# Kernel optimization log

Measured on AMD Instinct MI355X. Metric: run time of the kernel, lower is better.

The kernel has to match this reference:

```python
import jax, jax.numpy as jnp
import numpy as np

B, T, V, D, H, C = 256, 512, 400000, 50, 50, 5  # batch, seq, vocab, emb_dim, lstm_hidden, classes


def setup_inputs() -> dict:
    key = jax.random.key(0)
    ks = jax.random.split(key, 9)
    x = jax.random.randint(ks[0], (B, T), 0, V)
    lengths = jax.random.randint(ks[1], (B,), 1, T + 1)
    bows = jnp.zeros((B, 1), dtype=jnp.float32)  # unused by the model
    emb_table = jax.random.normal(ks[2], (V, D), dtype=jnp.float32) * 0.1
    s = 1.0 / np.sqrt(H)
    W_ih = jax.random.uniform(ks[3], (4 * H, D), minval=-s, maxval=s, dtype=jnp.float32)
    W_hh = jax.random.uniform(ks[4], (4 * H, H), minval=-s, maxval=s, dtype=jnp.float32)
    b_ih = jax.random.uniform(ks[5], (4 * H,), minval=-s, maxval=s, dtype=jnp.float32)
    b_hh = jax.random.uniform(ks[6], (4 * H,), minval=-s, maxval=s, dtype=jnp.float32)
    sl = 1.0 / np.sqrt(3 * H)
    W_lin = jax.random.uniform(ks[7], (C, 3 * H), minval=-sl, maxval=sl, dtype=jnp.float32)
    b_lin = jax.random.uniform(ks[8], (C,), minval=-sl, maxval=sl, dtype=jnp.float32)
    return {"x": x, "lengths": lengths, "bows": bows, "emb_table": emb_table,
            "W_ih": W_ih, "W_hh": W_hh, "b_ih": b_ih, "b_hh": b_hh,
            "W_lin": W_lin, "b_lin": b_lin}


def _lstm(emb, W_ih, W_hh, b_ih, b_hh):
    # emb: [B,T,D] -> h_all: [B,T,H]; PyTorch gate order i,f,g,o
    xp = jnp.einsum('btd,gd->btg', emb, W_ih) + b_ih + b_hh  # [B,T,4H]
    xp_t = jnp.swapaxes(xp, 0, 1)  # [T,B,4H]
    h0 = jnp.zeros((emb.shape[0], W_hh.shape[1]), emb.dtype)
    c0 = jnp.zeros_like(h0)

    def step(carry, xt):
        h, c = carry
        g = xt + h @ W_hh.T
        i, f, gg, o = jnp.split(g, 4, axis=-1)
        i, f, o = jax.nn.sigmoid(i), jax.nn.sigmoid(f), jax.nn.sigmoid(o)
        c = f * c + i * jnp.tanh(gg)
        h = o * jnp.tanh(c)
        return (h, c), h

    _, h_all = jax.lax.scan(step, (h0, c0), xp_t)
    return jnp.swapaxes(h_all, 0, 1)  # [B,T,H]


def reference(x, lengths, bows, emb_table, W_ih, W_hh, b_ih, b_hh, W_lin, b_lin):
    emb = emb_table[x]                              # [B,T,D]
    h_all = _lstm(emb, W_ih, W_hh, b_ih, b_hh)      # [B,T,H]
    idx = jnp.minimum(lengths, h_all.shape[1]) - 1  # last valid timestep
    last = jnp.take_along_axis(h_all, idx[:, None, None], axis=1)[:, 0, :]  # [B,H]
    # faithful to original: sum over full padded seq / length, max over full padded seq
    mean = jnp.sum(emb, axis=1) / lengths[:, None].astype(emb.dtype)        # [B,D]
    mx = jnp.max(emb, axis=1)                                               # [B,D]
    rep = jnp.concatenate([last, mean, mx], axis=1)                          # [B,3H]
    return rep @ W_lin.T + b_lin
```

## Files before the change

### kernel.cpp

```cpp
#include <hip/hip_runtime.h>
#include <cmath>

#define NB 256
#define NT 512
#define ND 50
#define NH 50
#define NC 5

typedef float f32x4 __attribute__((ext_vector_type(4)));
typedef float f32x2 __attribute__((ext_vector_type(2)));

__device__ __forceinline__ float rcpf(float x) { return __builtin_amdgcn_rcpf(x); }
__device__ __forceinline__ float rdl(float v, int l) {
    return __int_as_float(__builtin_amdgcn_readlane(__float_as_int(v), l));
}
__device__ __forceinline__ void gload4(f32x4& d, const float* p) {
    asm volatile("global_load_dwordx4 %0, %1, off" : "=v"(d) : "v"(p));
}

#define FENCE_BAR                                             \
    asm volatile("s_waitcnt lgkmcnt(0)" ::: "memory");        \
    __builtin_amdgcn_s_barrier();                             \
    asm volatile("" ::: "memory");

__global__ __launch_bounds__(256)
void k0_prep(const float* __restrict__ W_hh, const float* __restrict__ W_ih,
             float* __restrict__ wsWih, float* __restrict__ wsWhh)
{
    int idx = blockIdx.x * 256 + threadIdx.x;
    if (idx < 200 * 52) {
        int d = idx / 52, c = idx - (idx / 52) * 52;
        wsWih[idx] = (c < ND) ? W_ih[d * ND + c] : 0.f;
    } else if (idx < 2 * 200 * 52) {
        int j = idx - 200 * 52;
        int d = j / 52, c = j - (j / 52) * 52;
        wsWhh[j] = (c < NH) ? W_hh[d * NH + c] : 0.f;
    }
}

#define DECLROW(P) f32x4 P##_0{},P##_1{},P##_2{},P##_3{},P##_4{},P##_5{},P##_6{},P##_7{}, \
                         P##_8{},P##_9{},P##_10{},P##_11{},P##_12{};
#define LOADROW(P,B) { const float* b_=(B); \
    gload4(P##_0,b_+0);  gload4(P##_1,b_+4);  gload4(P##_2,b_+8);  gload4(P##_3,b_+12); \
    gload4(P##_4,b_+16); gload4(P##_5,b_+20); gload4(P##_6,b_+24); gload4(P##_7,b_+28); \
    gload4(P##_8,b_+32); gload4(P##_9,b_+36); gload4(P##_10,b_+40); gload4(P##_11,b_+44); \
    gload4(P##_12,b_+48); }

#define FMA2(H,W,A) __builtin_elementwise_fma((H),(W),(A))
#define KP2(J) { f32x2 a_=e0[2*(J)], b_=e0[2*(J)+1], c_=e1[2*(J)], d_=e1[2*(J)+1]; \
    A01=FMA2(a_,w##J.xy,A01); A23=FMA2(b_,w##J.zw,A23);                            \
    B01=FMA2(c_,w##J.xy,B01); B23=FMA2(d_,w##J.zw,B23); }

__global__ __launch_bounds__(256)
void k1_xproj(const int* __restrict__ x, const int* __restrict__ lengths,
              const float* __restrict__ emb_table,
              const float* __restrict__ wsWih, const float* __restrict__ b_ih,
              const float* __restrict__ b_hh,
              float* __restrict__ xp, int t0, int t1, int tiles, int tcAlloc)
{
    const int b    = blockIdx.x / tiles;
    const int tile = blockIdx.x % tiles;
    const int rt0  = t0 + tile * 64;
    if (rt0 >= t1) return;
    if (rt0 >= lengths[b]) return;
    const int nrows = min(64, t1 - rt0);

    const int tid = threadIdx.x;
    const int* xrow = x + (size_t)b * NT + rt0;

    float bsum = 0.f;
    const float* wrow = wsWih + tid * 52;
    f32x4 w0{},w1{},w2{},w3{},w4{},w5{},w6{},w7{},w8{},w9{},w10{},w11{},w12{};
    gload4(w0,wrow+0); gload4(w1,wrow+4); gload4(w2,wrow+8); gload4(w3,wrow+12);
    gload4(w4,wrow+16); gload4(w5,wrow+20); gload4(w6,wrow+24); gload4(w7,wrow+28);
    gload4(w8,wrow+32); gload4(w9,wrow+36); gload4(w10,wrow+40); gload4(w11,wrow+44);
    gload4(w12,wrow+48);
    if (tid < 200) bsum = b_ih[tid] + b_hh[tid];
    asm volatile("s_waitcnt vmcnt(0)" ::: "memory");
    __builtin_amdgcn_sched_barrier(0);

    if (tid < 200) {
        const int wr = 4 * (tid % NH) + (tid / NH);
        float* xpb = xp + ((size_t)b * tcAlloc + (rt0 - t0)) * 200 + wr;
        int xr0 = __builtin_amdgcn_readfirstlane(xrow[0]);
        int xr1 = __builtin_amdgcn_readfirstlane(xrow[1]);
        for (int row = 0; row < nrows; row += 2) {
            const f32x2* e0 = (const f32x2*)(emb_table + (size_t)xr0 * ND);
            const f32x2* e1 = (const f32x2*)(emb_table + (size_t)xr1 * ND);
            const int nr = (row + 2 < nrows) ? row + 2 : 0;
            int nx0 = __builtin_amdgcn_readfirstlane(xrow[nr]);
            int nx1 = __builtin_amdgcn_readfirstlane(xrow[nr + 1]);
            f32x2 A01 = {bsum, 0.f}, A23 = {0.f, 0.f};
            f32x2 B01 = {bsum, 0.f}, B23 = {0.f, 0.f};
            KP2(0) KP2(1) KP2(2) KP2(3) KP2(4) KP2(5)
            KP2(6) KP2(7) KP2(8) KP2(9) KP2(10) KP2(11)
            A01 = FMA2(e0[24], w12.xy, A01);
            B01 = FMA2(e1[24], w12.xy, B01);
            xpb[(size_t)row * 200]       = (A01.x + A01.y) + (A23.x + A23.y);
            xpb[(size_t)(row + 1) * 200] = (B01.x + B01.y) + (B23.x + B23.y);
            xr0 = nx0; xr1 = nx1;
        }
    }
}

#define CDOT1(SEED,OUT) { f32x2 A01 = {(SEED), 0.f}, A23 = {0.f, 0.f};        \
    A01=FMA2(hp0 ,CW_0.xy ,A01); A23=FMA2(hp1 ,CW_0.zw ,A23);                 \
    A01=FMA2(hp2 ,CW_1.xy ,A01); A23=FMA2(hp3 ,CW_1.zw ,A23);                 \
    A01=FMA2(hp4 ,CW_2.xy ,A01); A23=FMA2(hp5 ,CW_2.zw ,A23);                 \
    A01=FMA2(hp6 ,CW_3.xy ,A01); A23=FMA2(hp7 ,CW_3.zw ,A23);                 \
    A01=FMA2(hp8 ,CW_4.xy ,A01); A23=FMA2(hp9 ,CW_4.zw ,A23);                 \
    A01=FMA2(hp10,CW_5.xy ,A01); A23=FMA2(hp11,CW_5.zw ,A23);                 \
    A01=FMA2(hp12,CW_6.xy ,A01); A23=FMA2(hp13,CW_6.zw ,A23);                 \
    A01=FMA2(hp14,CW_7.xy ,A01); A23=FMA2(hp15,CW_7.zw ,A23);                 \
    A01=FMA2(hp16,CW_8.xy ,A01); A23=FMA2(hp17,CW_8.zw ,A23);                 \
    A01=FMA2(hp18,CW_9.xy ,A01); A23=FMA2(hp19,CW_9.zw ,A23);                 \
    A01=FMA2(hp20,CW_10.xy,A01); A23=FMA2(hp21,CW_10.zw,A23);                 \
    A01=FMA2(hp22,CW_11.xy,A01); A23=FMA2(hp23,CW_11.zw,A23);                 \
    A23=FMA2(hp24,CW_12.xy,A23);                                              \
    OUT = (A01.x + A01.y) + (A23.x + A23.y); }

#define SSTEP(XQ, S) {                                                        \
    f32x2 hp0 ={rdl(hv,0 ),rdl(hv,1 )}, hp1 ={rdl(hv,2 ),rdl(hv,3 )};         \
    f32x2 hp2 ={rdl(hv,4 ),rdl(hv,5 )}, hp3 ={rdl(hv,6 ),rdl(hv,7 )};         \
    f32x2 hp4 ={rdl(hv,8 ),rdl(hv,9 )}, hp5 ={rdl(hv,10),rdl(hv,11)};         \
    f32x2 hp6 ={rdl(hv,12),rdl(hv,13)}, hp7 ={rdl(hv,14),rdl(hv,15)};         \
    f32x2 hp8 ={rdl(hv,16),rdl(hv,17)}, hp9 ={rdl(hv,18),rdl(hv,19)};         \
    f32x2 hp10={rdl(hv,20),rdl(hv,21)}, hp11={rdl(hv,22),rdl(hv,23)};         \
    f32x2 hp12={rdl(hv,24),rdl(hv,25)}, hp13={rdl(hv,26),rdl(hv,27)};         \
    f32x2 hp14={rdl(hv,28),rdl(hv,29)}, hp15={rdl(hv,30),rdl(hv,31)};         \
    f32x2 hp16={rdl(hv,32),rdl(hv,33)}, hp17={rdl(hv,34),rdl(hv,35)};         \
    f32x2 hp18={rdl(hv,36),rdl(hv,37)}, hp19={rdl(hv,38),rdl(hv,39)};         \
    f32x2 hp20={rdl(hv,40),rdl(hv,41)}, hp21={rdl(hv,42),rdl(hv,43)};         \
    f32x2 hp22={rdl(hv,44),rdl(hv,45)}, hp23={rdl(hv,46),rdl(hv,47)};         \
    f32x2 hp24={rdl(hv,48),rdl(hv,49)};                                       \
    float gg;                                                                 \
    CDOT1(XQ, gg)                                                             \
    { int sn_ = (S) + 4; if (sn_ > nsteps - 1) sn_ = nsteps - 1;              \
      XQ = xpb[(size_t)sn_ * 200]; }                                          \
    float act = fmaf(rcpf(1.f + __expf(-sce * gg)), sce, ade);                \
    abuf[(S) & 1][wid][kln] = act;                                            \
    FENCE_BAR                                                                 \
    float i_ = abuf[(S) & 1][0][kln];                                         \
    float f_ = abuf[(S) & 1][1][kln];                                         \
    float gt = abuf[(S) & 1][2][kln];                                         \
    float o_ = abuf[(S) & 1][3][kln];                                         \
    cst = fmaf(f_, cst, i_ * gt);                                             \
    float th = fmaf(rcpf(1.f + __expf(-2.f * cst)), 2.f, -1.f);               \
    hv = o_ * th;                                                             \
    hkeep = (t0 + (S) == lastidx) ? hv : hkeep;                               \
}

__global__ __launch_bounds__(256)
__attribute__((amdgpu_waves_per_eu(1, 1)))
void k2_scan(const int* __restrict__ x, const int* __restrict__ lengths,
             const float* __restrict__ emb_table,
             const float* __restrict__ wsWhh, const float* __restrict__ xp,
             const float* __restrict__ W_lin, const float* __restrict__ b_lin,
             float* __restrict__ stH, float* __restrict__ stC, float* __restrict__ lastH,
             float* __restrict__ out, int t0, int t1, int tcAlloc)
{
    const int b   = blockIdx.x, tid = threadIdx.x;
    const int wid = tid >> 6;
    const int kln = tid & 63;
    const int kc  = (kln < NH) ? kln : NH - 1;

    __shared__ __align__(16) float abuf[2][4][64];
    __shared__ int xv[NT];
    __shared__ float ps[5][52], pm[5][52];
    __shared__ float rep[160];

    const int lastidx = min(lengths[b], NT) - 1;
    const int nsteps  = t1 - t0;

    float hv  = (t0 == 0) ? 0.f : stH[b * NH + kc];
    float cst = (t0 == 0) ? 0.f : stC[b * NH + kc];

    DECLROW(CW)
    LOADROW(CW, wsWhh + ((size_t)wid * NH + kc) * 52)
    asm volatile("s_waitcnt vmcnt(0)" ::: "memory");
    __builtin_amdgcn_sched_barrier(0);

    const float sce = (wid == 2) ? 2.f : 1.f;
    const float ade = (wid == 2) ? -1.f : 0.f;

    const float* xpb = xp + (size_t)b * tcAlloc * 200 + 4 * kc + wid;
    float xq0 = xpb[0];
    float xq1 = xpb[200];
    float xq2 = xpb[400];
    float xq3 = xpb[600];
    float hkeep = 0.f;

    for (int s4 = 0; s4 < nsteps; s4 += 4) {
        SSTEP(xq0, s4 + 0)
        SSTEP(xq1, s4 + 1)
        SSTEP(xq2, s4 + 2)
        SSTEP(xq3, s4 + 3)
    }

    if (wid == 0 && kln < NH) {
        stH[b * NH + kln] = hv;
        stC[b * NH + kln] = cst;
        if (lastidx >= t0 && lastidx < t1) lastH[b * NH + kln] = hkeep;
    }

    if (t1 == NT) {
        for (int i = tid; i < NT; i += 256) xv[i] = x[(size_t)b * NT + i];
        __syncthreads();
        const int g5 = tid / ND, d5 = tid - g5 * ND;
        if (tid < 250) {
            float s = 0.f, m = -INFINITY;
            #pragma unroll 4
            for (int t = g5; t < NT; t += 5) {
                float e = emb_table[(size_t)xv[t] * ND + d5];
                s += e; m = fmaxf(m, e);
            }
            ps[g5][d5] = s; pm[g5][d5] = m;
        }
        __syncthreads();
        if (tid < NH) {
            float s = ps[0][tid] + ps[1][tid] + ps[2][tid] + ps[3][tid] + ps[4][tid];
            float m = fmaxf(fmaxf(fmaxf(pm[0][tid], pm[1][tid]),
                                  fmaxf(pm[2][tid], pm[3][tid])), pm[4][tid]);
            rep[tid]          = (lastidx >= t0) ? hkeep : lastH[b * NH + tid];
            rep[NH + tid]     = s / (float)lengths[b];
            rep[2 * NH + tid] = m;
        }
        __syncthreads();
        if (tid < NC) {
            float acc = b_lin[tid];
            #pragma unroll 5
            for (int j = 0; j < 3 * NH; ++j)
                acc = fmaf(rep[j], W_lin[tid * 3 * NH + j], acc);
            out[(size_t)b * NC + tid] = acc;
        }
    }
}

extern "C" void kernel_launch(void* const* d_in, const int* in_sizes, int n_in,
                              void* d_out, int out_size, void* d_ws, size_t ws_size,
                              hipStream_t stream) {
    const int*   x     = (const int*)d_in[0];
    const int*   len   = (const int*)d_in[1];
    const float* emb   = (const float*)d_in[3];
    const float* W_ih  = (const float*)d_in[4];
    const float* W_hh  = (const float*)d_in[5];
    const float* b_ih  = (const float*)d_in[6];
    const float* b_hh  = (const float*)d_in[7];
    const float* W_lin = (const float*)d_in[8];
    const float* b_lin = (const float*)d_in[9];
    float* outp = (float*)d_out;

    float* stH   = (float*)d_ws;
    float* stC   = stH + NB * NH;
    float* lastH = stC + NB * NH;
    float* wsWih = (float*)((char*)d_ws + 160 * 1024);
    float* wsWhh = wsWih + 200 * 52;
    const size_t xpOff = 256 * 1024;
    float* xp = (float*)((char*)d_ws + xpOff);

    size_t avail = (ws_size > xpOff + 8192) ? ws_size - xpOff - 8192 : 0;
    int tc = (int)(avail / ((size_t)NB * 200 * sizeof(float)));
    tc &= ~3;
    if (tc > NT) tc = NT;
    if (tc < 4)  tc = 4;

    hipLaunchKernelGGL(k0_prep, dim3(82), dim3(256), 0, stream, W_hh, W_ih, wsWih, wsWhh);

    for (int t0 = 0; t0 < NT; t0 += tc) {
        const int t1 = min(NT, t0 + tc);
        const int tiles = (t1 - t0 + 63) / 64;
        hipLaunchKernelGGL(k1_xproj, dim3(NB * tiles), dim3(256), 0, stream,
                           x, len, emb, wsWih, b_ih, b_hh, xp, t0, t1, tiles, tc);
        hipLaunchKernelGGL(k2_scan, dim3(NB), dim3(256), 0, stream,
                           x, len, emb, wsWhh, xp, W_lin, b_lin,
                           stH, stC, lastH, outp, t0, t1, tc);
    }
}
```

Before: 249.0 us.

## Fuse embedding sum/max pooling into the input-projection kernel

Moves the mean/max pooling over the full padded sequence out of the tail of the serial scan kernel and into the parallel xproj kernel. Idle threads 200-249 of each tile block gather one embedding column per row and write per-tile partial sums and maxes to a workspace buffer. The scan kernel then only reduces the 8 partials. Tiles past the sequence length still launch, so pooling covers padding, but they skip the GEMV. This takes latency off the one-block-per-batch tail, at the cost of extra launched blocks and a larger workspace offset that may shrink the time-chunk size.

After: 256.6 us. 1.03x slower.

```diff
diff --git a/kernel.cpp b/kernel.cpp
--- a/kernel.cpp
+++ b/kernel.cpp
@@ -56,17 +56,21 @@
               const float* __restrict__ emb_table,
               const float* __restrict__ wsWih, const float* __restrict__ b_ih,
               const float* __restrict__ b_hh,
-              float* __restrict__ xp, int t0, int t1, int tiles, int tcAlloc)
+              float* __restrict__ xp, float* __restrict__ pool,
+              int t0, int t1, int tiles, int tcAlloc, int fullPool)
 {
     const int b    = blockIdx.x / tiles;
     const int tile = blockIdx.x % tiles;
     const int rt0  = t0 + tile * 64;
     if (rt0 >= t1) return;
-    if (rt0 >= lengths[b]) return;
+    if (!fullPool && rt0 >= lengths[b]) return;
     const int nrows = min(64, t1 - rt0);
 
     const int tid = threadIdx.x;
     const int* xrow = x + (size_t)b * NT + rt0;
+    const bool doGemv = (tid < 200) && (rt0 < lengths[b]);
+    const bool doPool = fullPool && (tid >= 200) && (tid < 250);
+    const int  pd = tid - 200;
 
     float bsum = 0.f;
     const float* wrow = wsWih + tid * 52;
@@ -79,17 +83,19 @@
     asm volatile("s_waitcnt vmcnt(0)" ::: "memory");
     __builtin_amdgcn_sched_barrier(0);
 
-    if (tid < 200) {
-        const int wr = 4 * (tid % NH) + (tid / NH);
-        float* xpb = xp + ((size_t)b * tcAlloc + (rt0 - t0)) * 200 + wr;
-        int xr0 = __builtin_amdgcn_readfirstlane(xrow[0]);
-        int xr1 = __builtin_amdgcn_readfirstlane(xrow[1]);
-        for (int row = 0; row < nrows; row += 2) {
-            const f32x2* e0 = (const f32x2*)(emb_table + (size_t)xr0 * ND);
-            const f32x2* e1 = (const f32x2*)(emb_table + (size_t)xr1 * ND);
-            const int nr = (row + 2 < nrows) ? row + 2 : 0;
-            int nx0 = __builtin_amdgcn_readfirstlane(xrow[nr]);
-            int nx1 = __builtin_amdgcn_readfirstlane(xrow[nr + 1]);
+    const int wr = 4 * ((tid % NH)) + (tid / NH);
+    float* xpb = xp + ((size_t)b * tcAlloc + (rt0 - t0)) * 200 + wr;
+    float ps = 0.f, pm = -INFINITY;
+
+    int xr0 = __builtin_amdgcn_readfirstlane(xrow[0]);
+    int xr1 = __builtin_amdgcn_readfirstlane(xrow[1]);
+    for (int row = 0; row < nrows; row += 2) {
+        const f32x2* e0 = (const f32x2*)(emb_table + (size_t)xr0 * ND);
+        const f32x2* e1 = (const f32x2*)(emb_table + (size_t)xr1 * ND);
+        const int nr = (row + 2 < nrows) ? row + 2 : 0;
+        int nx0 = __builtin_amdgcn_readfirstlane(xrow[nr]);
+        int nx1 = __builtin_amdgcn_readfirstlane(xrow[nr + 1]);
+        if (doGemv) {
             f32x2 A01 = {bsum, 0.f}, A23 = {0.f, 0.f};
             f32x2 B01 = {bsum, 0.f}, B23 = {0.f, 0.f};
             KP2(0) KP2(1) KP2(2) KP2(3) KP2(4) KP2(5)
@@ -98,8 +104,21 @@
             B01 = FMA2(e1[24], w12.xy, B01);
             xpb[(size_t)row * 200]       = (A01.x + A01.y) + (A23.x + A23.y);
             xpb[(size_t)(row + 1) * 200] = (B01.x + B01.y) + (B23.x + B23.y);
-            xr0 = nx0; xr1 = nx1;
         }
+        if (doPool) {
+            float ev0 = emb_table[(size_t)xr0 * ND + pd];
+            float ev1 = emb_table[(size_t)xr1 * ND + pd];
+            ps = ps + ev0; pm = fmaxf(pm, ev0);
+            ps = ps + ev1; pm = fmaxf(pm, ev1);
+        }
+        xr0 = nx0; xr1 = nx1;
+    }
+    if (doPool) {
+        const int ta = rt0 >> 6;
+        float* poolS = pool;
+        float* poolM = pool + (size_t)NB * 8 * 64;
+        poolS[((size_t)b * 8 + ta) * 64 + pd] = ps;
+        poolM[((size_t)b * 8 + ta) * 64 + pd] = pm;
     }
 }
 
@@ -155,9 +174,10 @@
 void k2_scan(const int* __restrict__ x, const int* __restrict__ lengths,
              const float* __restrict__ emb_table,
              const float* __restrict__ wsWhh, const float* __restrict__ xp,
+             const float* __restrict__ pool,
              const float* __restrict__ W_lin, const float* __restrict__ b_lin,
              float* __restrict__ stH, float* __restrict__ stC, float* __restrict__ lastH,
-             float* __restrict__ out, int t0, int t1, int tcAlloc)
+             float* __restrict__ out, int t0, int t1, int tcAlloc, int fullPool)
 {
     const int b   = blockIdx.x, tid = threadIdx.x;
     const int wid = tid >> 6;
@@ -204,34 +224,58 @@
     }
 
     if (t1 == NT) {
-        for (int i = tid; i < NT; i += 256) xv[i] = x[(size_t)b * NT + i];
-        __syncthreads();
-        const int g5 = tid / ND, d5 = tid - g5 * ND;
-        if (tid < 250) {
-            float s = 0.f, m = -INFINITY;
-            #pragma unroll 4
-            for (int t = g5; t < NT; t += 5) {
-                float e = emb_table[(size_t)xv[t] * ND + d5];
-                s += e; m = fmaxf(m, e);
-            }
-            ps[g5][d5] = s; pm[g5][d5] = m;
-        }
-        __syncthreads();
-        if (tid < NH) {
-            float s = ps[0][tid] + ps[1][tid] + ps[2][tid] + ps[3][tid] + ps[4][tid];
-            float m = fmaxf(fmaxf(fmaxf(pm[0][tid], pm[1][tid]),
-                                  fmaxf(pm[2][tid], pm[3][tid])), pm[4][tid]);
-            rep[tid]          = (lastidx >= t0) ? hkeep : lastH[b * NH + tid];
-            rep[NH + tid]     = s / (float)lengths[b];
-            rep[2 * NH + tid] = m;
-        }
-        __syncthreads();
-        if (tid < NC) {
-            float acc = b_lin[tid];
-            #pragma unroll 5
-            for (int j = 0; j < 3 * NH; ++j)
-                acc = fmaf(rep[j], W_lin[tid * 3 * NH + j], acc);
-            out[(size_t)b * NC + tid] = acc;
+        if (fullPool) {
+            if (tid < NH) {
+                const float* poolS = pool;
+                const float* poolM = pool + (size_t)NB * 8 * 64;
+                float s = 0.f, m = -INFINITY;
+                #pragma unroll
+                for (int ta = 0; ta < 8; ++ta) {
+                    s = s + poolS[((size_t)b * 8 + ta) * 64 + tid];
+                    m = fmaxf(m, poolM[((size_t)b * 8 + ta) * 64 + tid]);
+                }
+                rep[tid]          = (lastidx >= t0) ? hkeep : lastH[b * NH + tid];
+                rep[NH + tid]     = s / (float)lengths[b];
+                rep[2 * NH + tid] = m;
+            }
+            __syncthreads();
+            if (tid < NC) {
+                float acc = b_lin[tid];
+                #pragma unroll 5
+                for (int j = 0; j < 3 * NH; ++j)
+                    acc = fmaf(rep[j], W_lin[tid * 3 * NH + j], acc);
+                out[(size_t)b * NC + tid] = acc;
+            }
+        } else {
+            for (int i = tid; i < NT; i += 256) xv[i] = x[(size_t)b * NT + i];
+            __syncthreads();
+            const int g5 = tid / ND, d5 = tid - g5 * ND;
+            if (tid < 250) {
+                float s = 0.f, m = -INFINITY;
+                #pragma unroll 4
+                for (int t = g5; t < NT; t += 5) {
+                    float e = emb_table[(size_t)xv[t] * ND + d5];
+                    s += e; m = fmaxf(m, e);
+                }
+                ps[g5][d5] = s; pm[g5][d5] = m;
+            }
+            __syncthreads();
+            if (tid < NH) {
+                float s = ps[0][tid] + ps[1][tid] + ps[2][tid] + ps[3][tid] + ps[4][tid];
+                float m = fmaxf(fmaxf(fmaxf(pm[0][tid], pm[1][tid]),
+                                      fmaxf(pm[2][tid], pm[3][tid])), pm[4][tid]);
+                rep[tid]          = (lastidx >= t0) ? hkeep : lastH[b * NH + tid];
+                rep[NH + tid]     = s / (float)lengths[b];
+                rep[2 * NH + tid] = m;
+            }
+            __syncthreads();
+            if (tid < NC) {
+                float acc = b_lin[tid];
+                #pragma unroll 5
+                for (int j = 0; j < 3 * NH; ++j)
+                    acc = fmaf(rep[j], W_lin[tid * 3 * NH + j], acc);
+                out[(size_t)b * NC + tid] = acc;
+            }
         }
     }
 }
@@ -255,7 +299,8 @@
     float* lastH = stC + NB * NH;
     float* wsWih = (float*)((char*)d_ws + 160 * 1024);
     float* wsWhh = wsWih + 200 * 52;
-    const size_t xpOff = 256 * 1024;
+    float* pool  = (float*)((char*)d_ws + 256 * 1024);
+    const size_t xpOff = 256 * 1024 + 1024 * 1024;
     float* xp = (float*)((char*)d_ws + xpOff);
 
     size_t avail = (ws_size > xpOff + 8192) ? ws_size - xpOff - 8192 : 0;
@@ -263,6 +308,7 @@
     tc &= ~3;
     if (tc > NT) tc = NT;
     if (tc < 4)  tc = 4;
+    const int fullPool = (tc >= NT) ? 1 : 0;
 
     hipLaunchKernelGGL(k0_prep, dim3(82), dim3(256), 0, stream, W_hh, W_ih, wsWih, wsWhh);
 
@@ -270,9 +316,10 @@
         const int t1 = min(NT, t0 + tc);
         const int tiles = (t1 - t0 + 63) / 64;
         hipLaunchKernelGGL(k1_xproj, dim3(NB * tiles), dim3(256), 0, stream,
-                           x, len, emb, wsWih, b_ih, b_hh, xp, t0, t1, tiles, tc);
+                           x, len, emb, wsWih, b_ih, b_hh, xp, pool,
+                           t0, t1, tiles, tc, fullPool);
         hipLaunchKernelGGL(k2_scan, dim3(NB), dim3(256), 0, stream,
-                           x, len, emb, wsWhh, xp, W_lin, b_lin,
-                           stH, stC, lastH, outp, t0, t1, tc);
-    }
-}
+                           x, len, emb, wsWhh, xp, pool, W_lin, b_lin,
+                           stH, stC, lastH, outp, t0, t1, tc, fullPool);
+    }
+}
```

## Overlap embedding mean/max pooling with LSTM recurrence steps in scan kernel

Applied to the files above, without the earlier changes.

Moves the embedding sum/max pooling out of the serial epilogue and into the recurrent scan loop. Each step, one wave (round-robin by step index) accumulates one prefetched embedding row and issues the gather for the token four steps ahead, so the gather latency hides behind the latency-bound recurrence. Token ids are loaded into shared memory before the loop. The old epilogue is kept as a fallback when the workspace forces multiple time chunks. The cost is extra instructions and loads inside the critical recurrent step.

After: 295.7 us. +18.8%, slower.

```diff
diff --git a/kernel.cpp b/kernel.cpp
--- a/kernel.cpp
+++ b/kernel.cpp
@@ -119,7 +119,7 @@
     A23=FMA2(hp24,CW_12.xy,A23);                                              \
     OUT = (A01.x + A01.y) + (A23.x + A23.y); }
 
-#define SSTEP(XQ, S) {                                                        \
+#define SSTEP(XQ, S, TT) {                                                    \
     f32x2 hp0 ={rdl(hv,0 ),rdl(hv,1 )}, hp1 ={rdl(hv,2 ),rdl(hv,3 )};         \
     f32x2 hp2 ={rdl(hv,4 ),rdl(hv,5 )}, hp3 ={rdl(hv,6 ),rdl(hv,7 )};         \
     f32x2 hp4 ={rdl(hv,8 ),rdl(hv,9 )}, hp5 ={rdl(hv,10),rdl(hv,11)};         \
@@ -137,6 +137,13 @@
     CDOT1(XQ, gg)                                                             \
     { int sn_ = (S) + 4; if (sn_ > nsteps - 1) sn_ = nsteps - 1;              \
       XQ = xpb[(size_t)sn_ * 200]; }                                          \
+    if (doPool && wid == (TT)) {                                              \
+        float ev_ = evP;                                                      \
+        if (kln < ND) { psum = psum + ev_; pmax = fmaxf(pmax, ev_); }         \
+        int sx_ = (S) + 4; if (sx_ > NT - 1) sx_ = NT - 1;                    \
+        int tok_ = xls[sx_];                                                  \
+        evP = (kln < ND) ? emb_table[(size_t)tok_ * ND + kln] : 0.f;          \
+    }                                                                         \
     float act = fmaf(rcpf(1.f + __expf(-sce * gg)), sce, ade);                \
     abuf[(S) & 1][wid][kln] = act;                                            \
     FENCE_BAR                                                                 \
@@ -157,7 +164,7 @@
              const float* __restrict__ wsWhh, const float* __restrict__ xp,
              const float* __restrict__ W_lin, const float* __restrict__ b_lin,
              float* __restrict__ stH, float* __restrict__ stC, float* __restrict__ lastH,
-             float* __restrict__ out, int t0, int t1, int tcAlloc)
+             float* __restrict__ out, int t0, int t1, int tcAlloc, int fullPool)
 {
     const int b   = blockIdx.x, tid = threadIdx.x;
     const int wid = tid >> 6;
@@ -165,12 +172,14 @@
     const int kc  = (kln < NH) ? kln : NH - 1;
 
     __shared__ __align__(16) float abuf[2][4][64];
-    __shared__ int xv[NT];
+    __shared__ int xls[NT];
+    __shared__ float pbufS[4][64], pbufM[4][64];
     __shared__ float ps[5][52], pm[5][52];
     __shared__ float rep[160];
 
     const int lastidx = min(lengths[b], NT) - 1;
     const int nsteps  = t1 - t0;
+    const bool doPool = (fullPool != 0);
 
     float hv  = (t0 == 0) ? 0.f : stH[b * NH + kc];
     float cst = (t0 == 0) ? 0.f : stC[b * NH + kc];
@@ -182,6 +191,15 @@
 
     const float sce = (wid == 2) ? 2.f : 1.f;
     const float ade = (wid == 2) ? -1.f : 0.f;
+
+    for (int i = tid; i < NT; i += 256) xls[i] = x[(size_t)b * NT + i];
+    __syncthreads();
+
+    float psum = 0.f, pmax = -INFINITY, evP = 0.f;
+    if (doPool) {
+        int tok = xls[wid];
+        evP = (kln < ND) ? emb_table[(size_t)tok * ND + kln] : 0.f;
+    }
 
     const float* xpb = xp + (size_t)b * tcAlloc * 200 + 4 * kc + wid;
     float xq0 = xpb[0];
@@ -191,10 +209,10 @@
     float hkeep = 0.f;
 
     for (int s4 = 0; s4 < nsteps; s4 += 4) {
-        SSTEP(xq0, s4 + 0)
-        SSTEP(xq1, s4 + 1)
-        SSTEP(xq2, s4 + 2)
-        SSTEP(xq3, s4 + 3)
+        SSTEP(xq0, s4 + 0, 0)
+        SSTEP(xq1, s4 + 1, 1)
+        SSTEP(xq2, s4 + 2, 2)
+        SSTEP(xq3, s4 + 3, 3)
     }
 
     if (wid == 0 && kln < NH) {
@@ -204,34 +222,54 @@
     }
 
     if (t1 == NT) {
-        for (int i = tid; i < NT; i += 256) xv[i] = x[(size_t)b * NT + i];
-        __syncthreads();
-        const int g5 = tid / ND, d5 = tid - g5 * ND;
-        if (tid < 250) {
-            float s = 0.f, m = -INFINITY;
-            #pragma unroll 4
-            for (int t = g5; t < NT; t += 5) {
-                float e = emb_table[(size_t)xv[t] * ND + d5];
-                s += e; m = fmaxf(m, e);
-            }
-            ps[g5][d5] = s; pm[g5][d5] = m;
-        }
-        __syncthreads();
-        if (tid < NH) {
-            float s = ps[0][tid] + ps[1][tid] + ps[2][tid] + ps[3][tid] + ps[4][tid];
-            float m = fmaxf(fmaxf(fmaxf(pm[0][tid], pm[1][tid]),
-                                  fmaxf(pm[2][tid], pm[3][tid])), pm[4][tid]);
-            rep[tid]          = (lastidx >= t0) ? hkeep : lastH[b * NH + tid];
-            rep[NH + tid]     = s / (float)lengths[b];
-            rep[2 * NH + tid] = m;
-        }
-        __syncthreads();
-        if (tid < NC) {
-            float acc = b_lin[tid];
-            #pragma unroll 5
-            for (int j = 0; j < 3 * NH; ++j)
-                acc = fmaf(rep[j], W_lin[tid * 3 * NH + j], acc);
-            out[(size_t)b * NC + tid] = acc;
+        if (doPool) {
+            pbufS[wid][kln] = psum;
+            pbufM[wid][kln] = pmax;
+            __syncthreads();
+            if (tid < NH) {
+                float s = (pbufS[0][tid] + pbufS[1][tid]) + (pbufS[2][tid] + pbufS[3][tid]);
+                float m = fmaxf(fmaxf(pbufM[0][tid], pbufM[1][tid]),
+                                fmaxf(pbufM[2][tid], pbufM[3][tid]));
+                rep[tid]          = (lastidx >= t0) ? hkeep : lastH[b * NH + tid];
+                rep[NH + tid]     = s / (float)lengths[b];
+                rep[2 * NH + tid] = m;
+            }
+            __syncthreads();
+            if (tid < NC) {
+                float acc = b_lin[tid];
+                #pragma unroll 5
+                for (int j = 0; j < 3 * NH; ++j)
+                    acc = fmaf(rep[j], W_lin[tid * 3 * NH + j], acc);
+                out[(size_t)b * NC + tid] = acc;
+            }
+        } else {
+            const int g5 = tid / ND, d5 = tid - g5 * ND;
+            if (tid < 250) {
+                float s = 0.f, m = -INFINITY;
+                #pragma unroll 4
+                for (int t = g5; t < NT; t += 5) {
+                    float e = emb_table[(size_t)xls[t] * ND + d5];
+                    s += e; m = fmaxf(m, e);
+                }
+                ps[g5][d5] = s; pm[g5][d5] = m;
+            }
+            __syncthreads();
+            if (tid < NH) {
+                float s = ps[0][tid] + ps[1][tid] + ps[2][tid] + ps[3][tid] + ps[4][tid];
+                float m = fmaxf(fmaxf(fmaxf(pm[0][tid], pm[1][tid]),
+                                      fmaxf(pm[2][tid], pm[3][tid])), pm[4][tid]);
+                rep[tid]          = (lastidx >= t0) ? hkeep : lastH[b * NH + tid];
+                rep[NH + tid]     = s / (float)lengths[b];
+                rep[2 * NH + tid] = m;
+            }
+            __syncthreads();
+            if (tid < NC) {
+                float acc = b_lin[tid];
+                #pragma unroll 5
+                for (int j = 0; j < 3 * NH; ++j)
+                    acc = fmaf(rep[j], W_lin[tid * 3 * NH + j], acc);
+                out[(size_t)b * NC + tid] = acc;
+            }
         }
     }
 }
@@ -263,6 +301,7 @@
     tc &= ~3;
     if (tc > NT) tc = NT;
     if (tc < 4)  tc = 4;
+    const int fullPool = (tc >= NT) ? 1 : 0;
 
     hipLaunchKernelGGL(k0_prep, dim3(82), dim3(256), 0, stream, W_hh, W_ih, wsWih, wsWhh);
 
@@ -273,6 +312,6 @@
                            x, len, emb, wsWih, b_ih, b_hh, xp, t0, t1, tiles, tc);
         hipLaunchKernelGGL(k2_scan, dim3(NB), dim3(256), 0, stream,
                            x, len, emb, wsWhh, xp, W_lin, b_lin,
-                           stH, stC, lastH, outp, t0, t1, tc);
-    }
-}
+                           stH, stC, lastH, outp, t0, t1, tc, fullPool);
+    }
+}
```
